# Optimization experiments

Measured on AMD Instinct MI355X. Metric: run time of the kernel, lower is better.

Reference implementation:

```python
import jax, jax.numpy as jnp
import numpy as np

N_EMBD = 1024
HEAD_SIZE = 64
BLOCK_SIZE = 512
BATCH = 4


def setup_inputs() -> dict:
    key = jax.random.key(0)
    ks = jax.random.split(key, 5)
    T = BLOCK_SIZE
    x = jax.random.normal(ks[0], (BATCH, 2 * T - 1, N_EMBD), dtype=jnp.float32)
    scale = 1.0 / np.sqrt(N_EMBD)
    Wk = jax.random.normal(ks[1], (N_EMBD, HEAD_SIZE), dtype=jnp.float32) * scale
    Wv = jax.random.normal(ks[2], (N_EMBD, HEAD_SIZE), dtype=jnp.float32) * scale
    Wq = jax.random.normal(ks[3], (N_EMBD, HEAD_SIZE), dtype=jnp.float32) * scale
    # keyWindowBias in torch has shape (1,1,head_size,block_size); store as (hs, T)
    bias = jax.random.normal(ks[4], (HEAD_SIZE, T), dtype=jnp.float32)
    return {"x": x, "Wk": Wk, "Wv": Wv, "Wq": Wq, "bias": bias}


def reference(x, Wk, Wv, Wq, bias):
    B, S, C = x.shape
    T = (S + 1) // 2  # S == 2*T - 1 (block_size)
    xToPred = x[:, -T:, :]
    # block_layer == 0 path: project full sequence for k, v
    k = jnp.einsum('bsc,cd->bsd', x, Wk)        # [B, 2T-1, hs]
    v = jnp.einsum('bsc,cd->bsd', x, Wv)        # [B, 2T-1, hs]
    q = jnp.einsum('btc,cd->btd', xToPred, Wq)  # [B, T, hs]

    # sliding windows: window w covers positions w..w+T-1 (torch unfold semantics)
    idx = jnp.arange(T)[:, None] + jnp.arange(T)[None, :]  # [T, T]

    k_win = k[:, idx, :] + bias.T[None, None, :, :]  # [B, T, T, hs] + [1,1,T,hs]
    wei = jnp.einsum('bwd,bwtd->bwt', q, k_win)      # [B, T, T]
    wei = jax.nn.softmax(wei, axis=-1)

    v_win = v[:, idx, :]                              # [B, T, T, hs]
    out = jnp.einsum('bwt,bwtd->bwd', wei, v_win)     # [B, T, hs]
    return out
```

## Files before the change

### kernel.cpp

```cpp
#include <hip/hip_runtime.h>
#include <hip/hip_bf16.h>

#define BB 4
#define SS 1023
#define TT 512
#define CC 1024
#define DD 64
#define NROW (BB*SS)
#define NROWP 4096

typedef float f4 __attribute__((ext_vector_type(4)));
typedef float f2 __attribute__((ext_vector_type(2)));
typedef short bf16x8 __attribute__((ext_vector_type(8)));
typedef float f32x4 __attribute__((ext_vector_type(4)));

__device__ __forceinline__ unsigned split_rtn(float v) {
    const unsigned u  = __builtin_bit_cast(unsigned, v);
    const unsigned r  = u + 0x7FFFu + ((u >> 16) & 1u);
    const unsigned hi = r >> 16;
    const float hif   = __builtin_bit_cast(float, r & 0xFFFF0000u);
    const float res   = v - hif;
    const unsigned u2 = __builtin_bit_cast(unsigned, res);
    const unsigned r2 = u2 + 0x7FFFu + ((u2 >> 16) & 1u);
    return (r2 & 0xFFFF0000u) | hi;
}

__global__ __launch_bounds__(64) void split_kernel(
    const float* __restrict__ Wk,
    const float* __restrict__ Wv,
    const float* __restrict__ Wq,
    const float* __restrict__ x,
    unsigned short* __restrict__ bwh,
    unsigned short* __restrict__ bwl,
    unsigned short* __restrict__ xh,
    unsigned short* __restrict__ xl)
{
    const int lane = threadIdx.x;
    const int quad = lane >> 4, l4 = lane & 15;

    if (blockIdx.x < 384) {
        const int f    = blockIdx.x;
        const int p    = f >> 7;
        const int rem  = f & 127;
        const int nsub = rem >> 5;
        const int ks   = rem & 31;
        const float* W = (p == 0) ? Wk : (p == 1) ? Wv : Wq;
        const int n = nsub * 16 + l4;

        bf16x8 h, l;
#pragma unroll
        for (int j = 0; j < 8; ++j) {
            const int k = ks * 32 + quad * 8 + j;
            const unsigned hl = split_rtn(W[k * DD + n]);
            h[j] = (short)(hl & 0xFFFFu);
            l[j] = (short)(hl >> 16);
        }
        ((bf16x8*)bwh)[f * 64 + lane] = h;
        ((bf16x8*)bwl)[f * 64 + lane] = l;
    } else {
        const int mt = blockIdx.x - 384;
        int arow = mt * 16 + l4; if (arow > NROW - 1) arow = NROW - 1;
        const float* ap = x + (size_t)arow * CC;
        bf16x8* oh = (bf16x8*)xh + (size_t)(mt * 32) * 64 + lane;
        bf16x8* ol = (bf16x8*)xl + (size_t)(mt * 32) * 64 + lane;

#pragma unroll 4
        for (int ks = 0; ks < 32; ++ks) {
            const int k0 = ks * 32 + quad * 8;
            const f4 xa = *(const f4*)(ap + k0);
            const f4 xb = *(const f4*)(ap + k0 + 4);
            bf16x8 h, l;
#pragma unroll
            for (int j = 0; j < 4; ++j) {
                const unsigned hl = split_rtn(xa[j]);
                h[j] = (short)(hl & 0xFFFFu);
                l[j] = (short)(hl >> 16);
            }
#pragma unroll
            for (int j = 0; j < 4; ++j) {
                const unsigned hl = split_rtn(xb[j]);
                h[4 + j] = (short)(hl & 0xFFFFu);
                l[4 + j] = (short)(hl >> 16);
            }
            oh[ks * 64] = h;
            ol[ks * 64] = l;
        }
    }
}

__global__ __launch_bounds__(64) void proj_mfma_kernel(
    const unsigned short* __restrict__ xh,
    const unsigned short* __restrict__ xl,
    const unsigned short* __restrict__ bwh,
    const unsigned short* __restrict__ bwl,
    float* __restrict__ kT,
    float* __restrict__ vbuf,
    float* __restrict__ qbuf)
{
    const int blk  = blockIdx.x;
    const int p    = blk % 3;
    const int mt   = blk / 3;
    const int bs0  = mt * 16;
    const int lane = threadIdx.x;
    const int quad = lane >> 4, l4 = lane & 15;

    const bf16x8* xhp = (const bf16x8*)xh + (size_t)(mt * 32) * 64 + lane;
    const bf16x8* xlp = (const bf16x8*)xl + (size_t)(mt * 32) * 64 + lane;
    const bf16x8* bh  = (const bf16x8*)bwh + (size_t)(p * 4 * 32) * 64 + lane;
    const bf16x8* bl  = (const bf16x8*)bwl + (size_t)(p * 4 * 32) * 64 + lane;

    f32x4 acc[4];
#pragma unroll
    for (int n = 0; n < 4; ++n) acc[n] = (f32x4){0.f, 0.f, 0.f, 0.f};

#pragma unroll 2
    for (int ks = 0; ks < 32; ++ks) {
        const bf16x8 ah = xhp[ks * 64];
        const bf16x8 al = xlp[ks * 64];
#pragma unroll
        for (int n = 0; n < 4; ++n) {
            const bf16x8 bhn = bh[(n * 32 + ks) * 64];
            const bf16x8 bln = bl[(n * 32 + ks) * 64];
            acc[n] = __builtin_amdgcn_mfma_f32_16x16x32_bf16(ah, bhn, acc[n], 0, 0, 0);
            acc[n] = __builtin_amdgcn_mfma_f32_16x16x32_bf16(ah, bln, acc[n], 0, 0, 0);
            acc[n] = __builtin_amdgcn_mfma_f32_16x16x32_bf16(al, bhn, acc[n], 0, 0, 0);
            acc[n] = __builtin_amdgcn_mfma_f32_16x16x32_bf16(al, bln, acc[n], 0, 0, 0);
        }
    }

#pragma unroll
    for (int s = 0; s < 4; ++s) {
        const f32x4 a = acc[s];
        const int d = s * 16 + l4;
#pragma unroll
        for (int reg = 0; reg < 4; ++reg) {
            const int bs = bs0 + quad * 4 + reg;
            if (bs < NROW) {
                const float val = a[reg];
                const int b = bs / SS, ss = bs - b * SS;
                if (p == 0) {
                    kT[(size_t)d * NROWP + b * 1024 + ss] = val;
                } else if (p == 1) {
                    vbuf[(size_t)bs * DD + d] = val;
                } else {
                    if (ss >= TT - 1)
                        qbuf[((size_t)b * TT + (ss - (TT - 1))) * DD + d] = val;
                }
            }
        }
    }
}

__global__ __launch_bounds__(512) void attn_kernel(
    const float* __restrict__ kT,
    const float* __restrict__ vbuf,
    const float* __restrict__ qbuf,
    const float* __restrict__ bias,
    float* __restrict__ out)
{
    __shared__ __align__(8) float qsT[DD][2];
    __shared__ __align__(8) float part[2][2][TT];
    __shared__ __align__(8) float weiT[TT][2];
    __shared__ float red[16];
    __shared__ float invs[2];
    __shared__ float partial[8][2][DD];

    const int tid  = threadIdx.x;
    const int lane = tid & 63;
    const int wv   = tid >> 6;
    const int blk  = blockIdx.x;
    const int b    = blk >> 8;
    const int w0   = (blk & 255) * 2;

    if (tid < 2 * DD) {
        const int m = tid >> 6, dd = tid & 63;
        qsT[dd][m] = qbuf[((size_t)b * TT + w0 + m) * DD + dd];
    }
    __syncthreads();

    {
        const int h = tid >> 8, p = tid & 255;
        const int t0 = 2 * p;
        const float* kcol = kT + (size_t)(32 * h) * NROWP + b * 1024 + w0 + t0;
        const float* bp   = bias + (size_t)(32 * h) * TT + t0;
        float a00 = 0.f, a01 = 0.f, a10 = 0.f, a11 = 0.f;
#pragma unroll 8
        for (int i = 0; i < 32; ++i) {
            const float* kr = kcol + (size_t)i * NROWP;
            const f2 kA = *(const f2*)kr;
            const float kC = kr[2];
            const f2 bv = *(const f2*)(bp + (size_t)i * TT);
            const f2 qv = *(const f2*)&qsT[32 * h + i][0];
            a00 = fmaf(qv[0], kA[0], a00);
            a01 = fmaf(qv[0], kA[1], a01);
            a10 = fmaf(qv[1], kA[1], a10);
            a11 = fmaf(qv[1], kC,    a11);
            a00 = fmaf(qv[0], bv[0], a00);
            a01 = fmaf(qv[0], bv[1], a01);
            a10 = fmaf(qv[1], bv[0], a10);
            a11 = fmaf(qv[1], bv[1], a11);
        }
        *(f2*)&part[h][0][t0] = (f2){a00, a01};
        *(f2*)&part[h][1][t0] = (f2){a10, a11};
    }
    __syncthreads();

    {
        const int m = wv >> 2, qt = wv & 3;
        const int tb = qt * 128 + lane;
        float r0 = part[0][m][tb]      + part[1][m][tb];
        float r1 = part[0][m][tb + 64] + part[1][m][tb + 64];
        float mx = fmaxf(r0, r1);
#pragma unroll
        for (int off = 1; off < 64; off <<= 1)
            mx = fmaxf(mx, __shfl_xor(mx, off, 64));
        if (lane == 0) red[wv] = mx;
        __syncthreads();
        mx = fmaxf(fmaxf(red[m * 4], red[m * 4 + 1]),
                   fmaxf(red[m * 4 + 2], red[m * 4 + 3]));
        const float e0 = __expf(r0 - mx), e1 = __expf(r1 - mx);
        weiT[tb][m] = e0;
        weiT[tb + 64][m] = e1;
        float sum = e0 + e1;
#pragma unroll
        for (int off = 1; off < 64; off <<= 1)
            sum += __shfl_xor(sum, off, 64);
        if (lane == 0) red[8 + wv] = sum;
        __syncthreads();
        if (tid < 2)
            invs[tid] = 1.f / (red[8 + tid * 4] + red[9 + tid * 4] +
                               red[10 + tid * 4] + red[11 + tid * 4]);
    }
    __syncthreads();

    {
        const int t0r = wv * 64;
        const float* vb = vbuf + ((size_t)b * SS + w0 + t0r) * DD + lane;
        float p0 = 0.f, p1 = 0.f;
        float v0 = vb[0];
#pragma unroll 4
        for (int t = 0; t < 64; ++t) {
            const float v1 = vb[(size_t)(t + 1) * DD];
            const f2 w2 = *(const f2*)&weiT[t0r + t][0];
            p0 = fmaf(w2[0], v0, p0);
            p1 = fmaf(w2[1], v1, p1);
            v0 = v1;
        }
        partial[wv][0][lane] = p0;
        partial[wv][1][lane] = p1;
    }
    __syncthreads();

    if (tid < 2 * DD) {
        const int m = tid >> 6, dd = tid & 63;
        float o = 0.f;
#pragma unroll
        for (int j = 0; j < 8; ++j) o += partial[j][m][dd];
        out[((size_t)b * TT + w0 + m) * DD + dd] = o * invs[m];
    }
}

extern "C" void kernel_launch(void* const* d_in, const int* in_sizes, int n_in,
                              void* d_out, int out_size, void* d_ws, size_t ws_size,
                              hipStream_t stream) {
    const float* x    = (const float*)d_in[0];
    const float* Wk   = (const float*)d_in[1];
    const float* Wv   = (const float*)d_in[2];
    const float* Wq   = (const float*)d_in[3];
    const float* bias = (const float*)d_in[4];
    float* out = (float*)d_out;

    char* ws = (char*)d_ws;
    float* kT             = (float*)(ws + 0);
    float* vbuf           = (float*)(ws + (2u  << 20));
    float* qbuf           = (float*)(ws + (4u  << 20));
    unsigned short* bwh   = (unsigned short*)(ws + (6u  << 20));
    unsigned short* bwl   = (unsigned short*)(ws + (8u  << 20));
    unsigned short* xh    = (unsigned short*)(ws + (10u << 20));
    unsigned short* xl    = (unsigned short*)(ws + (20u << 20));

    split_kernel<<<640, 64, 0, stream>>>(Wk, Wv, Wq, x, bwh, bwl, xh, xl);
    proj_mfma_kernel<<<768, 64, 0, stream>>>(xh, xl, bwh, bwl, kT, vbuf, qbuf);
    attn_kernel<<<BB * TT / 2, 512, 0, stream>>>(kT, vbuf, qbuf, bias, out);
}
```

Baseline: 123.5 us.

## Fuse x bf16 split into projection kernel via swizzled LDS staging

```diff
diff --git a/kernel.cpp b/kernel.cpp
--- a/kernel.cpp
+++ b/kernel.cpp
@@ -12,6 +12,7 @@
 typedef float f4 __attribute__((ext_vector_type(4)));
 typedef float f2 __attribute__((ext_vector_type(2)));
 typedef short bf16x8 __attribute__((ext_vector_type(8)));
+typedef short s4 __attribute__((ext_vector_type(4)));
 typedef float f32x4 __attribute__((ext_vector_type(4)));
 
 __device__ __forceinline__ unsigned split_rtn(float v) {
@@ -25,118 +26,105 @@
     return (r2 & 0xFFFF0000u) | hi;
 }
 
-__global__ __launch_bounds__(64) void split_kernel(
+__global__ __launch_bounds__(64) void wsplit_kernel(
     const float* __restrict__ Wk,
     const float* __restrict__ Wv,
     const float* __restrict__ Wq,
-    const float* __restrict__ x,
     unsigned short* __restrict__ bwh,
-    unsigned short* __restrict__ bwl,
-    unsigned short* __restrict__ xh,
-    unsigned short* __restrict__ xl)
+    unsigned short* __restrict__ bwl)
 {
+    const int f    = blockIdx.x;
+    const int p    = f >> 7;
+    const int rem  = f & 127;
+    const int nsub = rem >> 5;
+    const int ks   = rem & 31;
     const int lane = threadIdx.x;
     const int quad = lane >> 4, l4 = lane & 15;
-
-    if (blockIdx.x < 384) {
-        const int f    = blockIdx.x;
-        const int p    = f >> 7;
-        const int rem  = f & 127;
-        const int nsub = rem >> 5;
-        const int ks   = rem & 31;
-        const float* W = (p == 0) ? Wk : (p == 1) ? Wv : Wq;
-        const int n = nsub * 16 + l4;
-
-        bf16x8 h, l;
-#pragma unroll
-        for (int j = 0; j < 8; ++j) {
-            const int k = ks * 32 + quad * 8 + j;
-            const unsigned hl = split_rtn(W[k * DD + n]);
-            h[j] = (short)(hl & 0xFFFFu);
-            l[j] = (short)(hl >> 16);
-        }
-        ((bf16x8*)bwh)[f * 64 + lane] = h;
-        ((bf16x8*)bwl)[f * 64 + lane] = l;
-    } else {
-        const int mt = blockIdx.x - 384;
-        int arow = mt * 16 + l4; if (arow > NROW - 1) arow = NROW - 1;
-        const float* ap = x + (size_t)arow * CC;
-        bf16x8* oh = (bf16x8*)xh + (size_t)(mt * 32) * 64 + lane;
-        bf16x8* ol = (bf16x8*)xl + (size_t)(mt * 32) * 64 + lane;
-
-#pragma unroll 4
-        for (int ks = 0; ks < 32; ++ks) {
-            const int k0 = ks * 32 + quad * 8;
-            const f4 xa = *(const f4*)(ap + k0);
-            const f4 xb = *(const f4*)(ap + k0 + 4);
-            bf16x8 h, l;
-#pragma unroll
-            for (int j = 0; j < 4; ++j) {
-                const unsigned hl = split_rtn(xa[j]);
-                h[j] = (short)(hl & 0xFFFFu);
-                l[j] = (short)(hl >> 16);
-            }
-#pragma unroll
-            for (int j = 0; j < 4; ++j) {
-                const unsigned hl = split_rtn(xb[j]);
-                h[4 + j] = (short)(hl & 0xFFFFu);
-                l[4 + j] = (short)(hl >> 16);
-            }
-            oh[ks * 64] = h;
-            ol[ks * 64] = l;
-        }
-    }
-}
-
-__global__ __launch_bounds__(64) void proj_mfma_kernel(
-    const unsigned short* __restrict__ xh,
-    const unsigned short* __restrict__ xl,
+    const float* W = (p == 0) ? Wk : (p == 1) ? Wv : Wq;
+    const int n = nsub * 16 + l4;
+
+    bf16x8 h, l;
+#pragma unroll
+    for (int j = 0; j < 8; ++j) {
+        const int k = ks * 32 + quad * 8 + j;
+        const unsigned hl = split_rtn(W[k * DD + n]);
+        h[j] = (short)(hl & 0xFFFFu);
+        l[j] = (short)(hl >> 16);
+    }
+    ((bf16x8*)bwh)[f * 64 + lane] = h;
+    ((bf16x8*)bwl)[f * 64 + lane] = l;
+}
+
+__global__ __launch_bounds__(256) void proj_fused_kernel(
+    const float* __restrict__ x,
     const unsigned short* __restrict__ bwh,
     const unsigned short* __restrict__ bwl,
     float* __restrict__ kT,
     float* __restrict__ vbuf,
     float* __restrict__ qbuf)
 {
+    __shared__ __align__(16) unsigned short lh[16 * 1024];
+    __shared__ __align__(16) unsigned short ll[16 * 1024];
+
     const int blk  = blockIdx.x;
     const int p    = blk % 3;
     const int mt   = blk / 3;
     const int bs0  = mt * 16;
-    const int lane = threadIdx.x;
+    const int tid  = threadIdx.x;
+
+    {
+        const int k = tid * 4;
+#pragma unroll 4
+        for (int i = 0; i < 16; ++i) {
+            int arow = bs0 + i; if (arow > NROW - 1) arow = NROW - 1;
+            const f4 xv = *(const f4*)(x + (size_t)arow * CC + k);
+            s4 h, l;
+#pragma unroll
+            for (int j = 0; j < 4; ++j) {
+                const unsigned hl = split_rtn(xv[j]);
+                h[j] = (short)(hl & 0xFFFFu);
+                l[j] = (short)(hl >> 16);
+            }
+            const int idx = i * 1024 + (k ^ ((i & 7) << 3));
+            *(s4*)&lh[idx] = h;
+            *(s4*)&ll[idx] = l;
+        }
+    }
+    __syncthreads();
+
+    const int lane = tid & 63;
+    const int w    = tid >> 6;
     const int quad = lane >> 4, l4 = lane & 15;
 
-    const bf16x8* xhp = (const bf16x8*)xh + (size_t)(mt * 32) * 64 + lane;
-    const bf16x8* xlp = (const bf16x8*)xl + (size_t)(mt * 32) * 64 + lane;
-    const bf16x8* bh  = (const bf16x8*)bwh + (size_t)(p * 4 * 32) * 64 + lane;
-    const bf16x8* bl  = (const bf16x8*)bwl + (size_t)(p * 4 * 32) * 64 + lane;
-
-    f32x4 acc[4];
-#pragma unroll
-    for (int n = 0; n < 4; ++n) acc[n] = (f32x4){0.f, 0.f, 0.f, 0.f};
-
-#pragma unroll 2
+    const bf16x8* bh = (const bf16x8*)bwh
+                     + (size_t)((p * 4 + w) * 32) * 64 + lane;
+    const bf16x8* bl = (const bf16x8*)bwl
+                     + (size_t)((p * 4 + w) * 32) * 64 + lane;
+
+    const int rbase = l4 * 1024;
+    const int kxor  = (l4 & 7) << 3;
+
+    f32x4 acc = {0.f, 0.f, 0.f, 0.f};
+#pragma unroll 4
     for (int ks = 0; ks < 32; ++ks) {
-        const bf16x8 ah = xhp[ks * 64];
-        const bf16x8 al = xlp[ks * 64];
-#pragma unroll
-        for (int n = 0; n < 4; ++n) {
-            const bf16x8 bhn = bh[(n * 32 + ks) * 64];
-            const bf16x8 bln = bl[(n * 32 + ks) * 64];
-            acc[n] = __builtin_amdgcn_mfma_f32_16x16x32_bf16(ah, bhn, acc[n], 0, 0, 0);
-            acc[n] = __builtin_amdgcn_mfma_f32_16x16x32_bf16(ah, bln, acc[n], 0, 0, 0);
-            acc[n] = __builtin_amdgcn_mfma_f32_16x16x32_bf16(al, bhn, acc[n], 0, 0, 0);
-            acc[n] = __builtin_amdgcn_mfma_f32_16x16x32_bf16(al, bln, acc[n], 0, 0, 0);
-        }
-    }
-
-#pragma unroll
-    for (int s = 0; s < 4; ++s) {
-        const f32x4 a = acc[s];
-        const int d = s * 16 + l4;
+        const int k0 = ks * 32 + quad * 8;
+        const bf16x8 ah = *(const bf16x8*)&lh[rbase + (k0 ^ kxor)];
+        const bf16x8 al = *(const bf16x8*)&ll[rbase + (k0 ^ kxor)];
+        const bf16x8 bhn = bh[ks * 64];
+        const bf16x8 bln = bl[ks * 64];
+        acc = __builtin_amdgcn_mfma_f32_16x16x32_bf16(ah, bhn, acc, 0, 0, 0);
+        acc = __builtin_amdgcn_mfma_f32_16x16x32_bf16(ah, bln, acc, 0, 0, 0);
+        acc = __builtin_amdgcn_mfma_f32_16x16x32_bf16(al, bhn, acc, 0, 0, 0);
+        acc = __builtin_amdgcn_mfma_f32_16x16x32_bf16(al, bln, acc, 0, 0, 0);
+    }
+
+    {
+        const int d = w * 16 + l4;
 #pragma unroll
         for (int reg = 0; reg < 4; ++reg) {
             const int bs = bs0 + quad * 4 + reg;
             if (bs < NROW) {
-                const float val = a[reg];
+                const float val = acc[reg];
                 const int b = bs / SS, ss = bs - b * SS;
                 if (p == 0) {
                     kT[(size_t)d * NROWP + b * 1024 + ss] = val;
@@ -276,10 +264,8 @@
     float* qbuf           = (float*)(ws + (4u  << 20));
     unsigned short* bwh   = (unsigned short*)(ws + (6u  << 20));
     unsigned short* bwl   = (unsigned short*)(ws + (8u  << 20));
-    unsigned short* xh    = (unsigned short*)(ws + (10u << 20));
-    unsigned short* xl    = (unsigned short*)(ws + (20u << 20));
-
-    split_kernel<<<640, 64, 0, stream>>>(Wk, Wv, Wq, x, bwh, bwl, xh, xl);
-    proj_mfma_kernel<<<768, 64, 0, stream>>>(xh, xl, bwh, bwl, kT, vbuf, qbuf);
+
+    wsplit_kernel<<<384, 64, 0, stream>>>(Wk, Wv, Wq, bwh, bwl);
+    proj_fused_kernel<<<768, 256, 0, stream>>>(x, bwh, bwl, kT, vbuf, qbuf);
     attn_kernel<<<BB * TT / 2, 512, 0, stream>>>(kT, vbuf, qbuf, bias, out);
 }
```

New measurement: 115.4 us. 1.07x faster.
